# Performance work log

Measured on AMD Instinct MI355X. Metric: run time of the kernel, lower is better.

The kernel has to match this reference:

```python
import jax, jax.numpy as jnp
import numpy as np

N_ENT, N_REL, H, DEG, TOPK = 150000, 500, 128, 32, 10


def setup_inputs() -> dict:
    key = jax.random.key(0)
    ks = jax.random.split(key, 8)
    return {
        "ent_emb": jax.random.normal(ks[0], (N_ENT, H), jnp.float32),
        "rel_emb": jax.random.normal(ks[1], (N_REL, H), jnp.float32),
        "W": jax.random.normal(ks[2], (H, H), jnp.float32) * 0.1,
        "W_r": jax.random.normal(ks[3], (H, H), jnp.float32) * 0.1,
        "a": jax.random.normal(ks[4], (3 * H, 1), jnp.float32) * 0.1,
        "neigh_w": jax.random.normal(ks[5], (H, H), jnp.float32) * 0.1,
        "src": jax.random.randint(ks[6], (N_ENT, DEG), 0, N_ENT),      # src node of each in-edge per dst
        "rel_id": jax.random.randint(ks[7], (N_ENT, DEG), 0, N_REL),   # relation id per edge
    }


def reference(ent_emb, rel_emb, W, W_r, a, neigh_w, src, rel_id):
    # node / relation projections
    h_node = ent_emb @ W                    # [N_ENT, H]
    h_rel = rel_emb @ W_r                   # [N_REL, H]
    # split attention vector: leaky_relu([h_src|h_dst|r] @ a) == leaky_relu(h_src@a1 + h_dst@a2 + r@a3)
    a1, a2, a3 = a[:H, 0], a[H:2 * H, 0], a[2 * H:, 0]
    s_src = h_node @ a1                     # [N_ENT]
    s_dst = h_node @ a2                     # [N_ENT]
    s_rel = h_rel @ a3                      # [N_REL]

    # edge scores on full graph; dst of row i is node i
    score = jax.nn.leaky_relu(s_src[src] + s_dst[:, None] + s_rel[rel_id], 0.2)  # [N_ENT, DEG]

    # top-k incoming edges per destination (dgl.sampling.select_topk, edge_dir='in')
    _, top_idx = jax.lax.top_k(score, TOPK)                 # [N_ENT, TOPK]
    src_k = jnp.take_along_axis(src, top_idx, axis=1)       # [N_ENT, TOPK]
    rel_k = jnp.take_along_axis(rel_id, top_idx, axis=1)

    # recompute attention on sampled subgraph + edge softmax per destination
    e = jax.nn.leaky_relu(s_src[src_k] + s_dst[:, None] + s_rel[rel_k], 0.2)     # [N_ENT, TOPK]
    attn = jax.nn.softmax(e, axis=1)

    # composition (add) of gathered src features with relation features, weighted scatter-sum
    comp = h_node[src_k] + h_rel[rel_k]                     # [N_ENT, TOPK, H]
    neigh = jnp.einsum('nkh,nk->nh', comp, attn)            # weighted sum over in-edges

    out = jnp.tanh(neigh @ neigh_w)                         # bn=None, dropout=eval identity
    return out
```

## Files before the change

### kernel.cpp

```cpp
#include <hip/hip_runtime.h>
#include <hip/hip_bf16.h>
#include <math.h>

#define N_ENT 150000
#define N_REL 500
#define H     128
#define DEG   32
#define TOPK  10

typedef unsigned short ushort_t;
typedef unsigned int   uint_t;
typedef __attribute__((ext_vector_type(8))) short short8;
typedef __attribute__((ext_vector_type(4))) float f32x4;

__device__ inline ushort_t f2bf(float x) {
    __hip_bfloat16 h = __float2bfloat16(x);
    return *reinterpret_cast<ushort_t*>(&h);
}
__device__ inline float bf2f(ushort_t u) {
    uint_t v = ((uint_t)u) << 16;
    return *reinterpret_cast<float*>(&v);
}
__device__ inline float dot4(float4 a, float4 b) {
    return a.x * b.x + a.y * b.y + a.z * b.z + a.w * b.w;
}
__device__ inline float fast_tanh(float x) {
    float e = __expf(2.f * x);
    return 1.f - 2.f * __builtin_amdgcn_rcpf(e + 1.f);
}

__global__ __launch_bounds__(128) void precompute_small(
    const float* __restrict__ W, const float* __restrict__ Wr,
    const float* __restrict__ nw, const float* __restrict__ a,
    float* __restrict__ M, float* __restrict__ M2,
    float* __restrict__ v1, float* __restrict__ v2, float* __restrict__ u3)
{
    int j = threadIdx.x;
    if (blockIdx.x < H) {
        int r = blockIdx.x;
        float m = 0.f, m2 = 0.f;
        for (int t = 0; t < H; ++t) {
            float x = nw[t * H + j];
            m  += W [r * H + t] * x;
            m2 += Wr[r * H + t] * x;
        }
        M [r * H + j] = m;
        M2[r * H + j] = m2;
    } else {
        int h = j;
        float s1 = 0.f, s2 = 0.f, s3 = 0.f;
        for (int t = 0; t < H; ++t) {
            s1 += W [h * H + t] * a[t];
            s2 += W [h * H + t] * a[H + t];
            s3 += Wr[h * H + t] * a[2 * H + t];
        }
        v1[h] = s1; v2[h] = s2; u3[h] = s3;
    }
}

__global__ __launch_bounds__(64) void bfrag_build(
    const float* __restrict__ M, ushort_t* __restrict__ Bhi,
    ushort_t* __restrict__ Blo)
{
    int b = blockIdx.x;
    int c = b >> 2, tt = b & 3;
    int l = threadIdx.x;
    int n  = c * 16 + (l & 15);
    int k0 = tt * 32 + (l >> 4) * 8;
    #pragma unroll
    for (int j = 0; j < 8; ++j) {
        float x = M[(k0 + j) * H + n];
        ushort_t h = f2bf(x);
        Bhi[(size_t)(b * 64 + l) * 8 + j] = h;
        Blo[(size_t)(b * 64 + l) * 8 + j] = f2bf(x - bf2f(h));
    }
}

__global__ __launch_bounds__(128) void rel_transform(
    const float* __restrict__ rel, const float* __restrict__ M2,
    const float* __restrict__ u3, ushort_t* __restrict__ Rb,
    float* __restrict__ srel)
{
    __shared__ float red[H];
    int r = blockIdx.x, j = threadIdx.x;
    float acc = 0.f;
    for (int h = 0; h < H; ++h)
        acc += rel[r * H + h] * M2[h * H + j];
    Rb[r * H + j] = f2bf(acc);
    red[j] = rel[r * H + j] * u3[j];
    __syncthreads();
    for (int s = 64; s > 0; s >>= 1) {
        if (j < s) red[j] += red[j + s];
        __syncthreads();
    }
    if (j == 0) srel[r] = red[0];
}

__global__ __launch_bounds__(256) void ent_transform3(
    const float* __restrict__ ent, const ushort_t* __restrict__ Bhi,
    const ushort_t* __restrict__ Blo, const float* __restrict__ v1,
    const float* __restrict__ v2, ushort_t* __restrict__ Gb,
    float* __restrict__ ssrc, float* __restrict__ sdst)
{
    const int t    = threadIdx.x;
    const int w    = t >> 6;
    const int l    = t & 63;
    const int m    = l & 15;
    const int quad = l >> 4;
    const long blockRow = (long)blockIdx.x * 128;
    const long waveRow  = blockRow + (long)w * 32;

    float4 v1a[4], v1b[4], v2a[4], v2b[4];
    #pragma unroll
    for (int tt = 0; tt < 4; ++tt) {
        const float* p1 = v1 + tt * 32 + quad * 8;
        const float* p2 = v2 + tt * 32 + quad * 8;
        v1a[tt] = *(const float4*)p1; v1b[tt] = *(const float4*)(p1 + 4);
        v2a[tt] = *(const float4*)p2; v2b[tt] = *(const float4*)(p2 + 4);
    }

    short8 Ahi[2][4], Alo[2][4];
    float p1s[2] = {0.f, 0.f}, p2s[2] = {0.f, 0.f};
    #pragma unroll
    for (int s = 0; s < 2; ++s) {
        long row = waveRow + s * 16 + m;
        long rc  = row < N_ENT ? row : (N_ENT - 1);
        const float* rp = ent + rc * H;
        #pragma unroll
        for (int tt = 0; tt < 4; ++tt) {
            float4 e0 = *(const float4*)(rp + tt * 32 + quad * 8);
            float4 e1 = *(const float4*)(rp + tt * 32 + quad * 8 + 4);
            p1s[s] += dot4(e0, v1a[tt]) + dot4(e1, v1b[tt]);
            p2s[s] += dot4(e0, v2a[tt]) + dot4(e1, v2b[tt]);
            float x[8] = {e0.x, e0.y, e0.z, e0.w, e1.x, e1.y, e1.z, e1.w};
            #pragma unroll
            for (int j = 0; j < 8; ++j) {
                ushort_t h = f2bf(x[j]);
                Ahi[s][tt][j] = (short)h;
                Alo[s][tt][j] = (short)f2bf(x[j] - bf2f(h));
            }
        }
    }
    #pragma unroll
    for (int s = 0; s < 2; ++s) {
        p1s[s] += __shfl_xor(p1s[s], 16); p1s[s] += __shfl_xor(p1s[s], 32);
        p2s[s] += __shfl_xor(p2s[s], 16); p2s[s] += __shfl_xor(p2s[s], 32);
    }
    if (quad == 0) {
        #pragma unroll
        for (int s = 0; s < 2; ++s) {
            long row = waveRow + s * 16 + m;
            if (row < N_ENT) { ssrc[row] = p1s[s]; sdst[row] = p2s[s]; }
        }
    }

    for (int c = 0; c < 8; ++c) {
        short8 bh[4], bl[4];
        #pragma unroll
        for (int tt = 0; tt < 4; ++tt) {
            size_t off = (size_t)((c * 4 + tt) * 64 + l) * 8;
            bh[tt] = *(const short8*)(Bhi + off);
            bl[tt] = *(const short8*)(Blo + off);
        }
        f32x4 acc0 = {0.f, 0.f, 0.f, 0.f}, acc1 = {0.f, 0.f, 0.f, 0.f};
        #pragma unroll
        for (int tt = 0; tt < 4; ++tt) {
            acc0 = __builtin_amdgcn_mfma_f32_16x16x32_bf16(Ahi[0][tt], bh[tt], acc0, 0, 0, 0);
            acc0 = __builtin_amdgcn_mfma_f32_16x16x32_bf16(Alo[0][tt], bh[tt], acc0, 0, 0, 0);
            acc0 = __builtin_amdgcn_mfma_f32_16x16x32_bf16(Ahi[0][tt], bl[tt], acc0, 0, 0, 0);
            acc1 = __builtin_amdgcn_mfma_f32_16x16x32_bf16(Ahi[1][tt], bh[tt], acc1, 0, 0, 0);
            acc1 = __builtin_amdgcn_mfma_f32_16x16x32_bf16(Alo[1][tt], bh[tt], acc1, 0, 0, 0);
            acc1 = __builtin_amdgcn_mfma_f32_16x16x32_bf16(Ahi[1][tt], bl[tt], acc1, 0, 0, 0);
        }
        #pragma unroll
        for (int s = 0; s < 2; ++s) {
            f32x4 a = s ? acc1 : acc0;
            #pragma unroll
            for (int r = 0; r < 4; ++r) {
                long row = waveRow + s * 16 + quad * 4 + r;
                if (row < N_ENT)
                    Gb[row * H + c * 16 + m] = f2bf(a[r]);
            }
        }
    }
}

__global__ __launch_bounds__(256) void gather_topk_out(
    const int* __restrict__ src, const int* __restrict__ rel_id,
    const float* __restrict__ ssrc, const float* __restrict__ sdst,
    const float* __restrict__ srel, const ushort_t* __restrict__ Gb,
    const ushort_t* __restrict__ Rb, float* __restrict__ out)
{
    const int l         = threadIdx.x & 31;
    const int halfShift = threadIdx.x & 32;
    int hw  = (blockIdx.x * blockDim.x + threadIdx.x) >> 5;
    int nhw = (gridDim.x * blockDim.x) >> 5;

    for (int i = hw; i < N_ENT; i += nhw) {
        int sidx = src   [(size_t)i * DEG + l];
        int ridx = rel_id[(size_t)i * DEG + l];
        float x   = ssrc[sidx] + sdst[i] + srel[ridx];
        float val = x >= 0.f ? x : 0.2f * x;

        int rank = 0;
        float mx = val;
        #pragma unroll
        for (int xm = 1; xm < 32; ++xm) {
            float v2 = __shfl_xor(val, xm, 32);
            bool ahead = (v2 > val) || (v2 == val && (l ^ xm) < l);
            rank += ahead ? 1 : 0;
            mx = fmaxf(mx, v2);
        }
        bool sel = rank < TOPK;

        float e  = sel ? __expf(val - mx) : 0.f;
        float ws = e;
        #pragma unroll
        for (int off = 1; off < 32; off <<= 1)
            ws += __shfl_xor(ws, off, 32);
        float w = e * __builtin_amdgcn_rcpf(ws);

        unsigned long long ball = __ballot(sel);
        uint_t mask = (uint_t)(ball >> halfShift);

        uint_t packed = (uint_t)sidx | ((uint_t)ridx << 18);
        uint_t pk[TOPK]; float wk[TOPK];
        #pragma unroll
        for (int k = 0; k < TOPK; ++k) {
            int lk = (int)__builtin_ctz(mask); mask &= mask - 1;
            pk[k] = (uint_t)__shfl((int)packed, lk, 32);
            wk[k] = __shfl(w, lk, 32);
        }

        ushort4 gv[TOPK], rv[TOPK];
        #pragma unroll
        for (int k = 0; k < TOPK; ++k) {
            size_t s_k = pk[k] & 0x3FFFF;
            size_t r_k = pk[k] >> 18;
            gv[k] = *(const ushort4*)(Gb + s_k * H + l * 4);
            rv[k] = *(const ushort4*)(Rb + r_k * H + l * 4);
        }
        float4 acc = {0.f, 0.f, 0.f, 0.f};
        #pragma unroll
        for (int k = 0; k < TOPK; ++k) {
            float wv = wk[k];
            acc.x += wv * (bf2f(gv[k].x) + bf2f(rv[k].x));
            acc.y += wv * (bf2f(gv[k].y) + bf2f(rv[k].y));
            acc.z += wv * (bf2f(gv[k].z) + bf2f(rv[k].z));
            acc.w += wv * (bf2f(gv[k].w) + bf2f(rv[k].w));
        }
        float4 o;
        o.x = fast_tanh(acc.x); o.y = fast_tanh(acc.y);
        o.z = fast_tanh(acc.z); o.w = fast_tanh(acc.w);
        ((float4*)(out + (size_t)i * H))[l] = o;
    }
}

extern "C" void kernel_launch(void* const* d_in, const int* in_sizes, int n_in,
                              void* d_out, int out_size, void* d_ws, size_t ws_size,
                              hipStream_t stream) {
    const float* ent = (const float*)d_in[0];
    const float* rel = (const float*)d_in[1];
    const float* W   = (const float*)d_in[2];
    const float* Wr  = (const float*)d_in[3];
    const float* a   = (const float*)d_in[4];
    const float* nw  = (const float*)d_in[5];
    const int*   src = (const int*)d_in[6];
    const int*   rid = (const int*)d_in[7];
    float* out = (float*)d_out;

    float* ws = (float*)d_ws;
    float*    M    = ws;
    float*    M2   = M    + 16384;
    float*    v1   = M2   + 16384;
    float*    v2   = v1   + 128;
    float*    u3   = v2   + 128;
    float*    srel = u3   + 128;
    float*    ssrc = srel + 512;
    float*    sdst = ssrc + 150016;
    ushort_t* Bhi  = (ushort_t*)(sdst + 150016);
    ushort_t* Blo  = Bhi + 16384;
    ushort_t* Rb   = Blo + 16384;
    ushort_t* Gb   = Rb  + 64000;

    precompute_small<<<H + 1, H, 0, stream>>>(W, Wr, nw, a, M, M2, v1, v2, u3);
    bfrag_build    <<<32, 64, 0, stream>>>(M, Bhi, Blo);
    rel_transform  <<<N_REL, H, 0, stream>>>(rel, M2, u3, Rb, srel);
    ent_transform3 <<<(N_ENT + 127) / 128, 256, 0, stream>>>(ent, Bhi, Blo,
                                                             v1, v2, Gb, ssrc, sdst);
    gather_topk_out<<<2048, 256, 0, stream>>>(src, rid, ssrc, sdst, srel,
                                              Gb, Rb, out);
}
```

Baseline: 326.4 us.

## Vectorize G stores, use integer sort keys for top-k rank, pack bf16 math

The projection kernel now swaps MFMA operands so each lane holds four consecutive columns of one row. That lets it write G as a single 8-byte ushort4 store instead of four scattered 2-byte stores. In the gather kernel, the top-k ranking loop switches from float compares with a tie-break to a single 64-bit key made of an order-preserving integer of the score plus the lane index. The max is tracked as that integer and converted back to float afterwards. The bf16 unpack and weighted sum now work on packed float2 vectors so the compiler can emit packed FP32 instructions.

```diff
diff --git a/kernel.cpp b/kernel.cpp
--- a/kernel.cpp
+++ b/kernel.cpp
@@ -12,6 +12,7 @@
 typedef unsigned int   uint_t;
 typedef __attribute__((ext_vector_type(8))) short short8;
 typedef __attribute__((ext_vector_type(4))) float f32x4;
+typedef __attribute__((ext_vector_type(2))) float f32x2;
 
 __device__ inline ushort_t f2bf(float x) {
     __hip_bfloat16 h = __float2bfloat16(x);
@@ -20,6 +21,14 @@
 __device__ inline float bf2f(ushort_t u) {
     uint_t v = ((uint_t)u) << 16;
     return *reinterpret_cast<float*>(&v);
+}
+__device__ inline f32x2 unpk2(uint_t u) {
+    uint_t lo = u << 16;
+    uint_t hi = u & 0xFFFF0000u;
+    f32x2 r;
+    r.x = *reinterpret_cast<float*>(&lo);
+    r.y = *reinterpret_cast<float*>(&hi);
+    return r;
 }
 __device__ inline float dot4(float4 a, float4 b) {
     return a.x * b.x + a.y * b.y + a.z * b.z + a.w * b.w;
@@ -165,21 +174,22 @@
         f32x4 acc0 = {0.f, 0.f, 0.f, 0.f}, acc1 = {0.f, 0.f, 0.f, 0.f};
         #pragma unroll
         for (int tt = 0; tt < 4; ++tt) {
-            acc0 = __builtin_amdgcn_mfma_f32_16x16x32_bf16(Ahi[0][tt], bh[tt], acc0, 0, 0, 0);
-            acc0 = __builtin_amdgcn_mfma_f32_16x16x32_bf16(Alo[0][tt], bh[tt], acc0, 0, 0, 0);
-            acc0 = __builtin_amdgcn_mfma_f32_16x16x32_bf16(Ahi[0][tt], bl[tt], acc0, 0, 0, 0);
-            acc1 = __builtin_amdgcn_mfma_f32_16x16x32_bf16(Ahi[1][tt], bh[tt], acc1, 0, 0, 0);
-            acc1 = __builtin_amdgcn_mfma_f32_16x16x32_bf16(Alo[1][tt], bh[tt], acc1, 0, 0, 0);
-            acc1 = __builtin_amdgcn_mfma_f32_16x16x32_bf16(Ahi[1][tt], bl[tt], acc1, 0, 0, 0);
+            acc0 = __builtin_amdgcn_mfma_f32_16x16x32_bf16(bh[tt], Ahi[0][tt], acc0, 0, 0, 0);
+            acc0 = __builtin_amdgcn_mfma_f32_16x16x32_bf16(bh[tt], Alo[0][tt], acc0, 0, 0, 0);
+            acc0 = __builtin_amdgcn_mfma_f32_16x16x32_bf16(bl[tt], Ahi[0][tt], acc0, 0, 0, 0);
+            acc1 = __builtin_amdgcn_mfma_f32_16x16x32_bf16(bh[tt], Ahi[1][tt], acc1, 0, 0, 0);
+            acc1 = __builtin_amdgcn_mfma_f32_16x16x32_bf16(bh[tt], Alo[1][tt], acc1, 0, 0, 0);
+            acc1 = __builtin_amdgcn_mfma_f32_16x16x32_bf16(bl[tt], Ahi[1][tt], acc1, 0, 0, 0);
         }
         #pragma unroll
         for (int s = 0; s < 2; ++s) {
             f32x4 a = s ? acc1 : acc0;
-            #pragma unroll
-            for (int r = 0; r < 4; ++r) {
-                long row = waveRow + s * 16 + quad * 4 + r;
-                if (row < N_ENT)
-                    Gb[row * H + c * 16 + m] = f2bf(a[r]);
+            long row = waveRow + s * 16 + m;
+            if (row < N_ENT) {
+                ushort4 o;
+                o.x = f2bf(a[0]); o.y = f2bf(a[1]);
+                o.z = f2bf(a[2]); o.w = f2bf(a[3]);
+                *(ushort4*)(Gb + (size_t)row * H + c * 16 + quad * 4) = o;
             }
         }
     }
@@ -193,6 +203,9 @@
 {
     const int l         = threadIdx.x & 31;
     const int halfShift = threadIdx.x & 32;
+    const uint_t tie1   = (uint_t)(31 - l);
+    const ushort_t* GbL = Gb + l * 4;
+    const ushort_t* RbL = Rb + l * 4;
     int hw  = (blockIdx.x * blockDim.x + threadIdx.x) >> 5;
     int nhw = (gridDim.x * blockDim.x) >> 5;
 
@@ -202,16 +215,24 @@
         float x   = ssrc[sidx] + sdst[i] + srel[ridx];
         float val = x >= 0.f ? x : 0.2f * x;
 
+        uint_t ub = __builtin_bit_cast(uint_t, val);
+        uint_t mk = ub ^ (uint_t)(((int)ub >> 31) | (int)0x80000000);
+        unsigned long long k1 = ((unsigned long long)mk << 5) | tie1;
+
         int rank = 0;
-        float mx = val;
+        uint_t mxk = mk;
         #pragma unroll
         for (int xm = 1; xm < 32; ++xm) {
-            float v2 = __shfl_xor(val, xm, 32);
-            bool ahead = (v2 > val) || (v2 == val && (l ^ xm) < l);
-            rank += ahead ? 1 : 0;
-            mx = fmaxf(mx, v2);
+            uint_t mk2 = (uint_t)__shfl_xor((int)mk, xm, 32);
+            unsigned long long k2 =
+                ((unsigned long long)mk2 << 5) | (tie1 ^ (uint_t)xm);
+            rank += (k2 > k1) ? 1 : 0;
+            mxk = mk2 > mxk ? mk2 : mxk;
         }
         bool sel = rank < TOPK;
+
+        uint_t mu = ((int)mxk < 0) ? (mxk ^ 0x80000000u) : ~mxk;
+        float mx = *reinterpret_cast<float*>(&mu);
 
         float e  = sel ? __expf(val - mx) : 0.f;
         float ws = e;
@@ -232,26 +253,26 @@
             wk[k] = __shfl(w, lk, 32);
         }
 
-        ushort4 gv[TOPK], rv[TOPK];
+        uint2 gv[TOPK], rv[TOPK];
         #pragma unroll
         for (int k = 0; k < TOPK; ++k) {
             size_t s_k = pk[k] & 0x3FFFF;
             size_t r_k = pk[k] >> 18;
-            gv[k] = *(const ushort4*)(Gb + s_k * H + l * 4);
-            rv[k] = *(const ushort4*)(Rb + r_k * H + l * 4);
-        }
-        float4 acc = {0.f, 0.f, 0.f, 0.f};
+            gv[k] = *(const uint2*)(GbL + s_k * H);
+            rv[k] = *(const uint2*)(RbL + r_k * H);
+        }
+        f32x2 a01 = {0.f, 0.f}, a23 = {0.f, 0.f};
         #pragma unroll
         for (int k = 0; k < TOPK; ++k) {
             float wv = wk[k];
-            acc.x += wv * (bf2f(gv[k].x) + bf2f(rv[k].x));
-            acc.y += wv * (bf2f(gv[k].y) + bf2f(rv[k].y));
-            acc.z += wv * (bf2f(gv[k].z) + bf2f(rv[k].z));
-            acc.w += wv * (bf2f(gv[k].w) + bf2f(rv[k].w));
+            f32x2 g01 = unpk2(gv[k].x), g23 = unpk2(gv[k].y);
+            f32x2 r01 = unpk2(rv[k].x), r23 = unpk2(rv[k].y);
+            a01 += (g01 + r01) * wv;
+            a23 += (g23 + r23) * wv;
         }
         float4 o;
-        o.x = fast_tanh(acc.x); o.y = fast_tanh(acc.y);
-        o.z = fast_tanh(acc.z); o.w = fast_tanh(acc.w);
+        o.x = fast_tanh(a01.x); o.y = fast_tanh(a01.y);
+        o.z = fast_tanh(a23.x); o.w = fast_tanh(a23.y);
         ((float4*)(out + (size_t)i * H))[l] = o;
     }
 }
```

Measured after the change: 328.9 us. About the same (+0.8%).
